# Kernel optimization log

Hardware: AMD Instinct MI355X
Metric: run time of the kernel (lower is better)

The kernel has to match this reference:

```python
import jax, jax.numpy as jnp
import numpy as np

B, S, D = 2, 2048, 2048          # batch, max_seq_len, hidden_dim_attention
G, HPG = 8, 4                    # n_head_groups, n_heads_per_group
H = G * HPG                      # total heads = 32
HD = D // H                      # head_dim = 64
KV = D // G                      # kv projection dim = 256
DFF = 5632                       # hidden_dim_feedforward
EPS = 1e-6
SCALE = 1.0 / (jnp.sqrt(jnp.float32(D // G)) + EPS)  # sqrt(attention_dim // n_head_groups) + eps


def setup_inputs() -> dict:
    key = jax.random.key(0)
    ks = jax.random.split(key, 12)
    s = lambda fan_in: 1.0 / np.sqrt(fan_in)
    return {
        "x": jax.random.normal(ks[0], (B, S, D), jnp.float32),
        "position_matrix": jax.random.uniform(ks[1], (2, 1, S, D), jnp.float32),
        "norm_attn_w": jnp.ones((D,), jnp.float32),
        "norm_ff_w": jnp.ones((D,), jnp.float32),
        "wq": jax.random.normal(ks[2], (D, D), jnp.float32) * s(D),
        "wk": jax.random.normal(ks[3], (KV, D), jnp.float32) * s(D),
        "wv": jax.random.normal(ks[4], (KV, D), jnp.float32) * s(D),
        "wo": jax.random.normal(ks[5], (D, D), jnp.float32) * s(D),
        "gate_w": jax.random.normal(ks[6], (DFF, D), jnp.float32) * s(D),
        "up_w": jax.random.normal(ks[7], (DFF, D), jnp.float32) * s(D),
        "down_w": jax.random.normal(ks[8], (DFF, D).__class__((D, DFF)), jnp.float32) * s(DFF),
    }


def rmsnorm(x, w):
    xf = x.astype(jnp.float32)
    n = xf / (jnp.sqrt(jnp.mean(xf * xf, axis=-1, keepdims=True) + EPS) + EPS)
    return n.astype(x.dtype) * w


def embed_position(x, pm):
    # faithful to source: rotated half times (cos + sin) tables (source multiplies _x by both)
    d = x.shape[-1]
    _x = jnp.concatenate((-x[..., d // 2:], x[..., :d // 2]), axis=-1)
    return (_x * pm[0][:, :, :d] + _x * pm[1][:, :, :d]).astype(x.dtype)


def block(x, position_matrix, norm_attn_w, norm_ff_w, wq, wk, wv, wo, gate_w, up_w, down_w):
    # ---- attention sublayer ----
    h = rmsnorm(x, norm_attn_w)
    xq = h @ wq.T                                   # [B,S,D]
    xk = h @ wk.T                                   # [B,S,KV]
    xv = h @ wv.T                                   # [B,S,KV]
    xq = embed_position(xq, position_matrix)
    xk = embed_position(xk, position_matrix)
    # GQA broadcast: each group's KV dims split into HPG heads of HD
    xk = jnp.broadcast_to(xk[:, :, None, :], (B, S, G, KV)).reshape(B, S, H, HD).transpose(0, 2, 1, 3)
    xv = jnp.broadcast_to(xv[:, :, None, :], (B, S, G, KV)).reshape(B, S, H, HD).transpose(0, 2, 1, 3)
    xq = xq.reshape(B, S, H, HD).transpose(0, 2, 1, 3)  # [B,H,S,HD]
    score = jnp.einsum("bhqd,bhkd->bhqk", xq, xk) * SCALE
    # source mask: strictly-upper triangle filled with 1e-10 (added, not -inf) -- faithful
    mask = jnp.triu(jnp.full((S, S), 1e-10, jnp.float32), k=1)
    score = score + mask
    e = jnp.exp(score.astype(jnp.float32))
    attn = (e / (jnp.sum(e, axis=-1, keepdims=True) + 1.0)).astype(xq.dtype)
    out = jnp.einsum("bhqk,bhkd->bhqd", attn, xv)
    out = out.transpose(0, 2, 1, 3).reshape(B, S, D) @ wo.T
    x = x + out
    # ---- feedforward sublayer (SwiGLU) ----
    h2 = rmsnorm(x, norm_ff_w)
    ff = (jax.nn.silu(h2 @ gate_w.T) * (h2 @ up_w.T)) @ down_w.T
    return x + ff


def reference(x, position_matrix, norm_attn_w, norm_ff_w, wq, wk, wv, wo, gate_w, up_w, down_w):
    return block(x, position_matrix, norm_attn_w, norm_ff_w, wq, wk, wv, wo, gate_w, up_w, down_w)
```

## Files before the change

kernel.cpp:

```cpp
#include <hip/hip_runtime.h>


typedef __attribute__((ext_vector_type(8))) __bf16 bf16x8;
typedef __attribute__((ext_vector_type(4))) __bf16 bf16x4;
typedef __attribute__((ext_vector_type(4))) float f32x4;

#define RR 4096
#define DD 2048
#define KVD 256
#define QKVN 2560
#define DFF 5632

static const size_t OFF_WQKV = 0;
static const size_t OFF_WO   = 10485760;
static const size_t OFF_WG   = 18874368;
static const size_t OFF_WU   = 41943040;
static const size_t OFF_WDN  = 65011712;
static const size_t OFF_H    = 88080384;
static const size_t OFF_QKV  = 104857600;
static const size_t OFF_Q    = 125829120;
static const size_t OFF_K    = 142606336;
static const size_t OFF_ACT  = 144703488;
static const size_t WS_NEED  = 190840832;

__device__ __forceinline__ void glds16(const __bf16* g, __bf16* s) {
  __builtin_amdgcn_global_load_lds(
      (const __attribute__((address_space(1))) unsigned int*)(const void*)g,
      (__attribute__((address_space(3))) unsigned int*)(void*)s, 16, 0, 0);
}

__global__ __launch_bounds__(256)
void cvt_all_kernel(const float* __restrict__ wq, const float* __restrict__ wk,
                    const float* __restrict__ wv, const float* __restrict__ wo,
                    const float* __restrict__ wg, const float* __restrict__ wu,
                    const float* __restrict__ wd, __bf16* __restrict__ wqkv,
                    __bf16* __restrict__ wob, __bf16* __restrict__ wgb,
                    __bf16* __restrict__ wub, __bf16* __restrict__ wdb) {
  int i = blockIdx.x * 256 + threadIdx.x;
  const float* s; __bf16* d; int si, di;
  if (i < 1048576)      { s = wq; d = wqkv; si = i;           di = i; }
  else if (i < 1179648) { s = wk; d = wqkv; si = i - 1048576; di = i; }
  else if (i < 1310720) { s = wv; d = wqkv; si = i - 1179648; di = i; }
  else if (i < 2359296) { s = wo; d = wob;  si = i - 1310720; di = si; }
  else if (i < 5242880) { s = wg; d = wgb;  si = i - 2359296; di = si; }
  else if (i < 8126464) { s = wu; d = wub;  si = i - 5242880; di = si; }
  else                  { s = wd; d = wdb;  si = i - 8126464; di = si; }
  float4 v = ((const float4*)s)[si];
  union { __bf16 b[4]; ushort4 u; } c;
  c.b[0] = (__bf16)v.x; c.b[1] = (__bf16)v.y; c.b[2] = (__bf16)v.z; c.b[3] = (__bf16)v.w;
  ((ushort4*)d)[di] = c.u;
}

__global__ __launch_bounds__(256)
void rmsnorm_kernel(const float* __restrict__ x, const float* __restrict__ w,
                    __bf16* __restrict__ out) {
  const int row = blockIdx.x, t = threadIdx.x;
  const float4* xr = (const float4*)(x + (size_t)row * DD);
  float4 a = xr[t], b = xr[t + 256];
  float s = a.x*a.x + a.y*a.y + a.z*a.z + a.w*a.w
          + b.x*b.x + b.y*b.y + b.z*b.z + b.w*b.w;
#pragma unroll
  for (int m = 1; m < 64; m <<= 1) s += __shfl_xor(s, m, 64);
  __shared__ float red[4];
  if ((t & 63) == 0) red[t >> 6] = s;
  __syncthreads();
  float tot = red[0] + red[1] + red[2] + red[3];
  float inv = 1.0f / (sqrtf(tot * (1.0f / 2048.0f) + 1e-6f) + 1e-6f);
  const float4* wr = (const float4*)w;
  float4 w0 = wr[t], w1 = wr[t + 256];
  __bf16* o = out + (size_t)row * DD;
  union { __bf16 bb[4]; ushort4 u; } c;
  c.bb[0] = (__bf16)(a.x*inv*w0.x); c.bb[1] = (__bf16)(a.y*inv*w0.y);
  c.bb[2] = (__bf16)(a.z*inv*w0.z); c.bb[3] = (__bf16)(a.w*inv*w0.w);
  ((ushort4*)o)[t] = c.u;
  c.bb[0] = (__bf16)(b.x*inv*w1.x); c.bb[1] = (__bf16)(b.y*inv*w1.y);
  c.bb[2] = (__bf16)(b.z*inv*w1.z); c.bb[3] = (__bf16)(b.w*inv*w1.w);
  ((ushort4*)o)[t + 256] = c.u;
}

template<int EPI>
__global__ __launch_bounds__(256)
void gemm_nt_kernel(const __bf16* __restrict__ A, const __bf16* __restrict__ Bm,
                    __bf16* Cb, const float* __restrict__ Res,
                    float* __restrict__ Cf, int M, int N, int K) {
  __shared__ __align__(16) __bf16 As[128 * 64];
  __shared__ __align__(16) __bf16 Bs[128 * 64];
  const int t = threadIdx.x;
  const int GM = M >> 7, GN = N >> 7;
  int m_t, n_t;
  if (GM == 32 && (GN & 3) == 0) {
    int lid = blockIdx.y * gridDim.x + blockIdx.x;
    int xcd = lid & 7, i = lid >> 3;
    int c = i >> 4, j = i & 15;
    m_t = xcd * 4 + (j & 3);
    n_t = c * 4 + (j >> 2);
  } else {
    m_t = blockIdx.y; n_t = blockIdx.x;
  }
  const int m0 = m_t * 128, n0 = n_t * 128;
  const int w = t >> 6, l = t & 63;
  const int wm = w & 1, wn = w >> 1;
  const int lm = l & 15, lq = l >> 4;
  const int srow = w * 8 + (l >> 3);
  const int sslot = (l & 7) ^ (l >> 3);
  const __bf16* Ap = A + (size_t)(m0 + srow) * K + sslot * 8;
  const __bf16* Bp = Bm + (size_t)(n0 + srow) * K + sslot * 8;
  __bf16* AsW = As + w * 512;
  __bf16* BsW = Bs + w * 512;
  const int sl0 = ((lq) ^ (lm & 7)) << 3;
  const int sl1 = ((4 + lq) ^ (lm & 7)) << 3;
  f32x4 acc[4][4] = {};
  for (int kt = 0; kt < K; kt += 64) {
    __syncthreads();
#pragma unroll
    for (int it = 0; it < 4; it++) {
      glds16(Ap + (size_t)(it * 32) * K + kt, AsW + it * 2048);
      glds16(Bp + (size_t)(it * 32) * K + kt, BsW + it * 2048);
    }
    __syncthreads();
    bf16x8 af[2][4], bfr[2][4];
#pragma unroll
    for (int i = 0; i < 4; i++) {
      af[0][i]  = *(const bf16x8*)&As[(wm * 64 + i * 16 + lm) * 64 + sl0];
      af[1][i]  = *(const bf16x8*)&As[(wm * 64 + i * 16 + lm) * 64 + sl1];
      bfr[0][i] = *(const bf16x8*)&Bs[(wn * 64 + i * 16 + lm) * 64 + sl0];
      bfr[1][i] = *(const bf16x8*)&Bs[(wn * 64 + i * 16 + lm) * 64 + sl1];
    }
#pragma unroll
    for (int kk = 0; kk < 2; kk++)
#pragma unroll
      for (int i = 0; i < 4; i++)
#pragma unroll
        for (int j = 0; j < 4; j++)
          acc[i][j] = __builtin_amdgcn_mfma_f32_16x16x32_bf16(af[kk][i], bfr[kk][j], acc[i][j], 0, 0, 0);
  }
#pragma unroll
  for (int i = 0; i < 4; i++)
#pragma unroll
    for (int j = 0; j < 4; j++)
#pragma unroll
      for (int r = 0; r < 4; r++) {
        int row = m0 + wm * 64 + i * 16 + lq * 4 + r;
        int col = n0 + wn * 64 + j * 16 + lm;
        size_t idx = (size_t)row * N + col;
        if (EPI == 0) {
          Cb[idx] = (__bf16)acc[i][j][r];
        } else {
          Cf[idx] = Res[idx] + acc[i][j][r];
        }
      }
}

__global__ __launch_bounds__(512)
void gemm_glu_kernel(const __bf16* __restrict__ A, const __bf16* __restrict__ Gm,
                     const __bf16* __restrict__ Um, __bf16* __restrict__ Cb,
                     int M, int N, int K) {
  __shared__ __align__(16) __bf16 As[128 * 64];
  __shared__ __align__(16) __bf16 Gs[128 * 64];
  __shared__ __align__(16) __bf16 Us[128 * 64];
  const int t = threadIdx.x, w = t >> 6, l = t & 63;
  const int lm = l & 15, lq = l >> 4;
  const int wm = w >> 2, wn = w & 3;
  const int lid = blockIdx.y * gridDim.x + blockIdx.x;
  const int xcd = lid & 7, i0 = lid >> 3;
  const int cc = i0 >> 4, jj0 = i0 & 15;
  const int m0 = (xcd * 4 + (jj0 & 3)) * 128;
  const int n0 = (cc * 4 + (jj0 >> 2)) * 128;
  const int srow = w * 8 + (l >> 3);
  const int sslot = (l & 7) ^ (l >> 3);
  const __bf16* Ap = A + (size_t)(m0 + srow) * K + sslot * 8;
  const __bf16* Gp = Gm + (size_t)(n0 + srow) * K + sslot * 8;
  const __bf16* Up = Um + (size_t)(n0 + srow) * K + sslot * 8;
  __bf16* AsW = As + w * 512;
  __bf16* GsW = Gs + w * 512;
  __bf16* UsW = Us + w * 512;
  const int sl0 = ((lq) ^ (lm & 7)) << 3;
  const int sl1 = ((4 + lq) ^ (lm & 7)) << 3;
  f32x4 accg[4][2] = {}, accu[4][2] = {};
  for (int kt = 0; kt < K; kt += 64) {
    __syncthreads();
    glds16(Ap + kt, AsW);
    glds16(Ap + (size_t)64 * K + kt, AsW + 4096);
    glds16(Gp + kt, GsW);
    glds16(Gp + (size_t)64 * K + kt, GsW + 4096);
    glds16(Up + kt, UsW);
    glds16(Up + (size_t)64 * K + kt, UsW + 4096);
    __syncthreads();
#pragma unroll
    for (int kk = 0; kk < 2; kk++) {
      const int sl = kk ? sl1 : sl0;
      bf16x8 af[4], bg[2], bu[2];
#pragma unroll
      for (int i = 0; i < 4; i++)
        af[i] = *(const bf16x8*)&As[(wm * 64 + i * 16 + lm) * 64 + sl];
#pragma unroll
      for (int j = 0; j < 2; j++) {
        bg[j] = *(const bf16x8*)&Gs[(wn * 32 + j * 16 + lm) * 64 + sl];
        bu[j] = *(const bf16x8*)&Us[(wn * 32 + j * 16 + lm) * 64 + sl];
      }
#pragma unroll
      for (int i = 0; i < 4; i++)
#pragma unroll
        for (int j = 0; j < 2; j++) {
          accg[i][j] = __builtin_amdgcn_mfma_f32_16x16x32_bf16(af[i], bg[j], accg[i][j], 0, 0, 0);
          accu[i][j] = __builtin_amdgcn_mfma_f32_16x16x32_bf16(af[i], bu[j], accu[i][j], 0, 0, 0);
        }
    }
  }
#pragma unroll
  for (int i = 0; i < 4; i++)
#pragma unroll
    for (int j = 0; j < 2; j++)
#pragma unroll
      for (int r = 0; r < 4; r++) {
        int row = m0 + wm * 64 + i * 16 + lq * 4 + r;
        int col = n0 + wn * 32 + j * 16 + lm;
        float g = accg[i][j][r];
        Cb[(size_t)row * N + col] = (__bf16)(g / (1.0f + __expf(-g)) * accu[i][j][r]);
      }
}

__global__ __launch_bounds__(256)
void rope_kernel(const __bf16* __restrict__ qkv, const float* __restrict__ pm,
                 __bf16* __restrict__ qo, __bf16* __restrict__ ko) {
  const int row = blockIdx.x, t = threadIdx.x;
  const int s = row & 2047;
  const __bf16* q = qkv + (size_t)row * QKVN;
  const float* p0 = pm + (size_t)s * DD;
  const float* p1 = p0 + (size_t)2048 * DD;
  __bf16* qr = qo + (size_t)row * DD;
#pragma unroll
  for (int jj = 0; jj < 8; jj++) {
    int i = t + jj * 256;
    float rot = (i < 1024) ? -(float)q[i + 1024] : (float)q[i - 1024];
    qr[i] = (__bf16)(rot * (p0[i] + p1[i]));
  }
  const __bf16* k = q + 2048;
  __bf16* kr = ko + (size_t)row * KVD;
  {
    int i = t;
    float rot = (i < 128) ? -(float)k[i + 128] : (float)k[i - 128];
    kr[i] = (__bf16)(rot * (p0[i] + p1[i]));
  }
}

__global__ __launch_bounds__(256)
void vt_kernel(const __bf16* __restrict__ qkv, __bf16* __restrict__ vt) {
  __shared__ __bf16 sT[64][264];
  const int t = threadIdx.x;
  const int kb = blockIdx.x, b = blockIdx.y;
  const int r = t & 63;
  const int c0 = t >> 6;
  const __bf16* src = qkv + ((size_t)(b * 2048 + kb * 64 + r)) * QKVN + 2304;
#pragma unroll
  for (int i = 0; i < 8; i++) {
    int c = c0 + i * 4;
    *(uint4*)&sT[r][c * 8] = *(const uint4*)(src + c * 8);
  }
  __syncthreads();
  __bf16* dst = vt + ((size_t)(b * 256 + t)) * 2048 + kb * 64;
  uint4 o[8];
  unsigned* ou = (unsigned*)o;
#pragma unroll
  for (int j = 0; j < 32; j++) {
    unsigned lo = *(const unsigned short*)&sT[2 * j][t];
    unsigned hi = *(const unsigned short*)&sT[2 * j + 1][t];
    ou[j] = lo | (hi << 16);
  }
#pragma unroll
  for (int i = 0; i < 8; i++) ((uint4*)dst)[i] = o[i];
}

__global__ __launch_bounds__(256)
void attn_kernel(const __bf16* __restrict__ Q, const __bf16* __restrict__ Kb,
                 const __bf16* __restrict__ Vt, __bf16* __restrict__ O) {
  __shared__ __align__(16) __bf16 sQ[128 * 72];
  __shared__ __align__(16) __bf16 sK[64 * 72];
  __shared__ __align__(16) __bf16 sV[64 * 72];
  __shared__ float sDen[128];
  const int t = threadIdx.x, l = t & 63, w = t >> 6;
  const int lm = l & 15, lq = l >> 4;
  const int q0 = blockIdx.x * 128;
  const int h = blockIdx.y, b = blockIdx.z;
  const int p = h & 3;
  const float scale = 1.0f / (16.0f + 1e-6f);
  {
    const int qr = t >> 3, qc = (t & 7) * 8;
#pragma unroll
    for (int it = 0; it < 4; it++) {
      size_t base = ((size_t)(b * 2048 + q0 + qr + it * 32)) * DD + h * 64 + qc;
      *(uint4*)&sQ[(qr + it * 32) * 72 + qc] = *(const uint4*)(Q + base);
    }
  }
  __syncthreads();
  bf16x8 bQ[2][2];
#pragma unroll
  for (int q_j = 0; q_j < 2; q_j++)
#pragma unroll
    for (int kk = 0; kk < 2; kk++)
      bQ[q_j][kk] = *(const bf16x8*)&sQ[(w * 32 + q_j * 16 + lm) * 72 + kk * 32 + lq * 8];
  f32x4 oacc[2][4] = {};
  float dsum[2] = {0.f, 0.f};
  const int ksr = t >> 2, ksc = (t & 3) * 16;
  const __bf16* vrow = Vt + ((size_t)(b * 256 + p * 64 + l)) * 2048 + w * 16;
  for (int kt = 0; kt < 2048; kt += 64) {
    const __bf16* krow = Kb + ((size_t)(b * 2048 + kt + ksr)) * KVD + p * 64 + ksc;
    uint4 kv0 = *(const uint4*)(krow);
    uint4 kv1 = *(const uint4*)(krow + 8);
    uint4 vv0 = *(const uint4*)(vrow + kt);
    uint4 vv1 = *(const uint4*)(vrow + kt + 8);
    __syncthreads();
    *(uint4*)&sK[ksr * 72 + ksc] = kv0;
    *(uint4*)&sK[ksr * 72 + ksc + 8] = kv1;
    *(uint4*)&sV[l * 72 + w * 16] = vv0;
    *(uint4*)&sV[l * 72 + w * 16 + 8] = vv1;
    __syncthreads();
#pragma unroll
    for (int kt2 = 0; kt2 < 2; kt2++) {
      union { bf16x8 v; __bf16 e[8]; } pA[2];
#pragma unroll
      for (int c = 0; c < 2; c++) {
        const int kt_i = kt2 * 2 + c;
        f32x4 sacc[2] = {};
#pragma unroll
        for (int kk = 0; kk < 2; kk++) {
          bf16x8 aK = *(const bf16x8*)&sK[(kt_i * 16 + lm) * 72 + kk * 32 + lq * 8];
#pragma unroll
          for (int q_j = 0; q_j < 2; q_j++)
            sacc[q_j] = __builtin_amdgcn_mfma_f32_16x16x32_bf16(aK, bQ[q_j][kk], sacc[q_j], 0, 0, 0);
        }
#pragma unroll
        for (int q_j = 0; q_j < 2; q_j++)
#pragma unroll
          for (int r = 0; r < 4; r++) {
            float e = __expf(sacc[q_j][r] * scale);
            dsum[q_j] += e;
            pA[q_j].e[c * 4 + r] = (__bf16)e;
          }
      }
#pragma unroll
      for (int d_n = 0; d_n < 4; d_n++) {
        union { bf16x8 v; bf16x4 h[2]; } bV;
        const __bf16* vb = &sV[(d_n * 16 + lm) * 72 + kt2 * 32 + lq * 4];
        bV.h[0] = *(const bf16x4*)(vb);
        bV.h[1] = *(const bf16x4*)(vb + 16);
#pragma unroll
        for (int q_j = 0; q_j < 2; q_j++)
          oacc[q_j][d_n] = __builtin_amdgcn_mfma_f32_16x16x32_bf16(pA[q_j].v, bV.v, oacc[q_j][d_n], 0, 0, 0);
      }
    }
  }
#pragma unroll
  for (int q_j = 0; q_j < 2; q_j++) {
    dsum[q_j] += __shfl_xor(dsum[q_j], 16, 64);
    dsum[q_j] += __shfl_xor(dsum[q_j], 32, 64);
  }
  if (l < 16) {
    sDen[w * 32 + l] = dsum[0];
    sDen[w * 32 + 16 + l] = dsum[1];
  }
  __syncthreads();
#pragma unroll
  for (int q_j = 0; q_j < 2; q_j++)
#pragma unroll
    for (int d_n = 0; d_n < 4; d_n++)
#pragma unroll
      for (int r = 0; r < 4; r++) {
        int rloc = w * 32 + q_j * 16 + lq * 4 + r;
        int row = q0 + rloc;
        int col = h * 64 + d_n * 16 + lm;
        O[((size_t)(b * 2048 + row)) * DD + col] = (__bf16)(oacc[q_j][d_n][r] / (sDen[rloc] + 1.0f));
      }
}

extern "C" void kernel_launch(void* const* d_in, const int* in_sizes, int n_in,
                              void* d_out, int out_size, void* d_ws, size_t ws_size,
                              hipStream_t stream) {
  if (ws_size < WS_NEED) return;

  const float* x    = (const float*)d_in[0];
  const float* pm   = (const float*)d_in[1];
  const float* w_na = (const float*)d_in[2];
  const float* w_nf = (const float*)d_in[3];
  const float* wq   = (const float*)d_in[4];
  const float* wk   = (const float*)d_in[5];
  const float* wv   = (const float*)d_in[6];
  const float* wo   = (const float*)d_in[7];
  const float* wg   = (const float*)d_in[8];
  const float* wu   = (const float*)d_in[9];
  const float* wd   = (const float*)d_in[10];

  char* ws = (char*)d_ws;
  __bf16* wqkv_b = (__bf16*)(ws + OFF_WQKV);
  __bf16* wo_b   = (__bf16*)(ws + OFF_WO);
  __bf16* wg_b   = (__bf16*)(ws + OFF_WG);
  __bf16* wu_b   = (__bf16*)(ws + OFF_WU);
  __bf16* wdn_b  = (__bf16*)(ws + OFF_WDN);
  __bf16* h_b    = (__bf16*)(ws + OFF_H);
  __bf16* qkv_b  = (__bf16*)(ws + OFF_QKV);
  __bf16* q_b    = (__bf16*)(ws + OFF_Q);
  __bf16* k_b    = (__bf16*)(ws + OFF_K);
  __bf16* act_b  = (__bf16*)(ws + OFF_ACT);
  float*  x1     = (float*)d_out;

  cvt_all_kernel<<<43008, 256, 0, stream>>>(wq, wk, wv, wo, wg, wu, wd,
                                            wqkv_b, wo_b, wg_b, wu_b, wdn_b);

  rmsnorm_kernel<<<4096, 256, 0, stream>>>(x, w_na, h_b);
  gemm_nt_kernel<0><<<dim3(20, 32), 256, 0, stream>>>(h_b, wqkv_b, qkv_b, nullptr, nullptr,
                                                      RR, QKVN, DD);
  rope_kernel<<<4096, 256, 0, stream>>>(qkv_b, pm, q_b, k_b);
  vt_kernel<<<dim3(32, 2), 256, 0, stream>>>(qkv_b, act_b);
  attn_kernel<<<dim3(16, 32, 2), 256, 0, stream>>>(q_b, k_b, act_b, h_b);
  gemm_nt_kernel<1><<<dim3(16, 32), 256, 0, stream>>>(h_b, wo_b, nullptr, x, x1,
                                                      RR, DD, DD);
  rmsnorm_kernel<<<4096, 256, 0, stream>>>(x1, w_nf, q_b);
  gemm_glu_kernel<<<dim3(44, 32), 512, 0, stream>>>(q_b, wg_b, wu_b, act_b,
                                                    RR, DFF, DD);
  gemm_nt_kernel<1><<<dim3(16, 32), 256, 0, stream>>>(act_b, wdn_b, nullptr, x1, x1,
                                                      RR, DD, DFF);
}
```

Measured before the change: 805.0 us.

## Enlarge NT GEMM tile to 128x256 with eight waves per block

The generic NT GEMM tile grows from 128x128 with 4 waves to 128x256 with 8 waves. Each wave still computes a 64x64 sub-tile, but each staged A tile is now reused across twice as many output columns, so global and LDS traffic per FLOP drops. Fragment loads are split per k-half, which lowers live registers. Grids for the QKV, output and down projections are halved to about one block per CU, and the XCD-aware tile mapping is now hardcoded for M=4096. The trade-off is fewer blocks to hide latency and more LDS per block.

```diff
diff --git a/kernel.cpp b/kernel.cpp
--- a/kernel.cpp
+++ b/kernel.cpp
@@ -79,28 +79,19 @@
 }
 
 template<int EPI>
-__global__ __launch_bounds__(256)
+__global__ __launch_bounds__(512)
 void gemm_nt_kernel(const __bf16* __restrict__ A, const __bf16* __restrict__ Bm,
                     __bf16* Cb, const float* __restrict__ Res,
                     float* __restrict__ Cf, int M, int N, int K) {
   __shared__ __align__(16) __bf16 As[128 * 64];
-  __shared__ __align__(16) __bf16 Bs[128 * 64];
-  const int t = threadIdx.x;
-  const int GM = M >> 7, GN = N >> 7;
-  int m_t, n_t;
-  if (GM == 32 && (GN & 3) == 0) {
-    int lid = blockIdx.y * gridDim.x + blockIdx.x;
-    int xcd = lid & 7, i = lid >> 3;
-    int c = i >> 4, j = i & 15;
-    m_t = xcd * 4 + (j & 3);
-    n_t = c * 4 + (j >> 2);
-  } else {
-    m_t = blockIdx.y; n_t = blockIdx.x;
-  }
-  const int m0 = m_t * 128, n0 = n_t * 128;
-  const int w = t >> 6, l = t & 63;
-  const int wm = w & 1, wn = w >> 1;
+  __shared__ __align__(16) __bf16 Bs[256 * 64];
+  const int t = threadIdx.x, w = t >> 6, l = t & 63;
   const int lm = l & 15, lq = l >> 4;
+  const int wm = w >> 2, wn = w & 3;
+  const int lid = blockIdx.y * gridDim.x + blockIdx.x;
+  const int xcd = lid & 7, i0 = lid >> 3;
+  const int m0 = (xcd * 4 + (i0 & 3)) * 128;
+  const int n0 = (i0 >> 2) * 256;
   const int srow = w * 8 + (l >> 3);
   const int sslot = (l & 7) ^ (l >> 3);
   const __bf16* Ap = A + (size_t)(m0 + srow) * K + sslot * 8;
@@ -112,27 +103,29 @@
   f32x4 acc[4][4] = {};
   for (int kt = 0; kt < K; kt += 64) {
     __syncthreads();
-#pragma unroll
-    for (int it = 0; it < 4; it++) {
-      glds16(Ap + (size_t)(it * 32) * K + kt, AsW + it * 2048);
-      glds16(Bp + (size_t)(it * 32) * K + kt, BsW + it * 2048);
+    glds16(Ap + kt, AsW);
+    glds16(Ap + (size_t)64 * K + kt, AsW + 4096);
+    glds16(Bp + kt, BsW);
+    glds16(Bp + (size_t)64 * K + kt, BsW + 4096);
+    glds16(Bp + (size_t)128 * K + kt, BsW + 8192);
+    glds16(Bp + (size_t)192 * K + kt, BsW + 12288);
+    __syncthreads();
+#pragma unroll
+    for (int kk = 0; kk < 2; kk++) {
+      const int sl = kk ? sl1 : sl0;
+      bf16x8 af[4], bfr[4];
+#pragma unroll
+      for (int i = 0; i < 4; i++)
+        af[i] = *(const bf16x8*)&As[(wm * 64 + i * 16 + lm) * 64 + sl];
+#pragma unroll
+      for (int j = 0; j < 4; j++)
+        bfr[j] = *(const bf16x8*)&Bs[(wn * 64 + j * 16 + lm) * 64 + sl];
+#pragma unroll
+      for (int i = 0; i < 4; i++)
+#pragma unroll
+        for (int j = 0; j < 4; j++)
+          acc[i][j] = __builtin_amdgcn_mfma_f32_16x16x32_bf16(af[i], bfr[j], acc[i][j], 0, 0, 0);
     }
-    __syncthreads();
-    bf16x8 af[2][4], bfr[2][4];
-#pragma unroll
-    for (int i = 0; i < 4; i++) {
-      af[0][i]  = *(const bf16x8*)&As[(wm * 64 + i * 16 + lm) * 64 + sl0];
-      af[1][i]  = *(const bf16x8*)&As[(wm * 64 + i * 16 + lm) * 64 + sl1];
-      bfr[0][i] = *(const bf16x8*)&Bs[(wn * 64 + i * 16 + lm) * 64 + sl0];
-      bfr[1][i] = *(const bf16x8*)&Bs[(wn * 64 + i * 16 + lm) * 64 + sl1];
-    }
-#pragma unroll
-    for (int kk = 0; kk < 2; kk++)
-#pragma unroll
-      for (int i = 0; i < 4; i++)
-#pragma unroll
-        for (int j = 0; j < 4; j++)
-          acc[i][j] = __builtin_amdgcn_mfma_f32_16x16x32_bf16(af[kk][i], bfr[kk][j], acc[i][j], 0, 0, 0);
   }
 #pragma unroll
   for (int i = 0; i < 4; i++)
@@ -407,16 +400,16 @@
                                             wqkv_b, wo_b, wg_b, wu_b, wdn_b);
 
   rmsnorm_kernel<<<4096, 256, 0, stream>>>(x, w_na, h_b);
-  gemm_nt_kernel<0><<<dim3(20, 32), 256, 0, stream>>>(h_b, wqkv_b, qkv_b, nullptr, nullptr,
+  gemm_nt_kernel<0><<<dim3(10, 32), 512, 0, stream>>>(h_b, wqkv_b, qkv_b, nullptr, nullptr,
                                                       RR, QKVN, DD);
   rope_kernel<<<4096, 256, 0, stream>>>(qkv_b, pm, q_b, k_b);
   vt_kernel<<<dim3(32, 2), 256, 0, stream>>>(qkv_b, act_b);
   attn_kernel<<<dim3(16, 32, 2), 256, 0, stream>>>(q_b, k_b, act_b, h_b);
-  gemm_nt_kernel<1><<<dim3(16, 32), 256, 0, stream>>>(h_b, wo_b, nullptr, x, x1,
-                                                      RR, DD, DD);
+  gemm_nt_kernel<1><<<dim3(8, 32), 512, 0, stream>>>(h_b, wo_b, nullptr, x, x1,
+                                                     RR, DD, DD);
   rmsnorm_kernel<<<4096, 256, 0, stream>>>(x1, w_nf, q_b);
   gemm_glu_kernel<<<dim3(44, 32), 512, 0, stream>>>(q_b, wg_b, wu_b, act_b,
                                                     RR, DFF, DD);
-  gemm_nt_kernel<1><<<dim3(16, 32), 256, 0, stream>>>(act_b, wdn_b, nullptr, x1, x1,
-                                                      RR, DD, DFF);
-}
+  gemm_nt_kernel<1><<<dim3(8, 32), 512, 0, stream>>>(act_b, wdn_b, nullptr, x1, x1,
+                                                     RR, DD, DFF);
+}
```

Result: slower. 825.5 us (+2.5%).
